# Kernel tuning notes

Hardware: AMD Instinct MI355X
Metric: run time of the kernel (lower is better)

The kernel has to match this reference:

```python
import jax, jax.numpy as jnp
import numpy as np

EMBED_DIM = 1024
NUM_HEADS = 16
HEAD_DIM = EMBED_DIM // NUM_HEADS
LAMBDA_ENTANGLE = 0.35


def setup_inputs() -> dict:
    key = jax.random.key(0)
    ks = jax.random.split(key, 10)
    B, S, D = 2, 2048, EMBED_DIM
    init = 1.0 / np.sqrt(D)  # mimic nn.Linear uniform init scale
    x = jax.random.normal(ks[0], (B, S, D), dtype=jnp.float32)
    Wq = jax.random.uniform(ks[1], (D, D), jnp.float32, -init, init)
    bq = jax.random.uniform(ks[2], (D,), jnp.float32, -init, init)
    Wk = jax.random.uniform(ks[3], (D, D), jnp.float32, -init, init)
    bk = jax.random.uniform(ks[4], (D,), jnp.float32, -init, init)
    Wv = jax.random.uniform(ks[5], (D, D), jnp.float32, -init, init)
    bv = jax.random.uniform(ks[6], (D,), jnp.float32, -init, init)
    Wo = jax.random.uniform(ks[7], (D, D), jnp.float32, -init, init)
    bo = jax.random.uniform(ks[8], (D,), jnp.float32, -init, init)
    J_attn = jax.random.normal(ks[9], (NUM_HEADS, HEAD_DIM, HEAD_DIM), dtype=jnp.float32) * 0.02
    lambda_attn = jnp.asarray(LAMBDA_ENTANGLE, dtype=jnp.float32)
    return {"x": x, "Wq": Wq, "bq": bq, "Wk": Wk, "bk": bk, "Wv": Wv, "bv": bv,
            "Wo": Wo, "bo": bo, "J_attn": J_attn, "lambda_attn": lambda_attn}


def reference(x, Wq, bq, Wk, bk, Wv, bv, Wo, bo, J_attn, lambda_attn):
    B, S, D = x.shape
    H, Hd = NUM_HEADS, HEAD_DIM
    scale = jnp.sqrt(jnp.asarray(Hd, dtype=x.dtype))

    def heads(W, b):
        # (B,S,D) @ (D,D) + b -> (B,H,S,Hd)
        y = jnp.einsum('bsd,ed->bse', x, W) + b
        return y.reshape(B, S, H, Hd).transpose(0, 2, 1, 3)

    Q = heads(Wq, bq)
    K = heads(Wk, bk)
    V = heads(Wv, bv)

    scores = jnp.einsum('bhid,bhjd->bhij', Q, K) / scale
    # bilinear entanglement correction: tanh(Q) J tanh(K)^T
    QJ = jnp.einsum('bhid,hde->bhie', jnp.tanh(Q), J_attn)  # (B,H,S,Hd)
    delta = jnp.einsum('bhie,bhje->bhij', QJ, jnp.tanh(K))
    scores = scores + lambda_attn * delta

    causal = jnp.triu(jnp.ones((S, S), dtype=bool), k=1)
    scores = jnp.where(causal, -jnp.inf, scores)

    probs = jax.nn.softmax(scores, axis=-1)
    out = jnp.einsum('bhij,bhjd->bhid', probs, V)  # (B,H,S,Hd)
    out = out.transpose(0, 2, 1, 3).reshape(B, S, D)
    return jnp.einsum('bsd,ed->bse', out, Wo) + bo
```

## Files before the change

kernel.cpp:

```cpp
#include <hip/hip_runtime.h>
#include <hip/hip_bf16.h>

typedef unsigned short u16;
typedef __bf16 bf16x8 __attribute__((ext_vector_type(8)));
typedef float f32x4 __attribute__((ext_vector_type(4)));
typedef unsigned short u16x4 __attribute__((ext_vector_type(4)));

#define MFMA16(a, b, c) __builtin_amdgcn_mfma_f32_16x16x32_bf16(a, b, c, 0, 0, 0)

#define EMB 1024
#define SEQ 2048
#define NH 16
#define HD 64
#define LOG2E 1.4426950408889634f

#define GLOAD_LDS16(g, l) __builtin_amdgcn_global_load_lds( \
    (const __attribute__((address_space(1))) unsigned int*)(g), \
    (__attribute__((address_space(3))) unsigned int*)(l), 16, 0, 0)

__device__ __forceinline__ float b2f(u16 u) {
    union { unsigned int i; float f; } v; v.i = ((unsigned int)u) << 16; return v.f;
}
__device__ __forceinline__ u16 f2b(float f) {
    __hip_bfloat16 h = __float2bfloat16(f);
    return *reinterpret_cast<u16*>(&h);
}
__device__ __forceinline__ u16x4 pack4(float a, float b, float c, float d) {
    union { __hip_bfloat162 h2[2]; u16x4 u; } r;
    r.h2[0] = __float22bfloat162_rn(float2{a, b});
    r.h2[1] = __float22bfloat162_rn(float2{c, d});
    return r.u;
}
__device__ __forceinline__ bf16x8 ldfrag(const u16* p) {
    return *reinterpret_cast<const bf16x8*>(p);
}
__device__ __forceinline__ bf16x8 cvt8(const float* p) {
    const float4 a = *reinterpret_cast<const float4*>(p);
    const float4 b = *reinterpret_cast<const float4*>(p + 4);
    union { u16x4 q[2]; bf16x8 v; } r;
    r.q[0] = pack4(a.x, a.y, a.z, a.w);
    r.q[1] = pack4(b.x, b.y, b.z, b.w);
    return r.v;
}
__device__ __forceinline__ float fast_tanh(float x) {
    float t = __builtin_amdgcn_exp2f(x * (2.0f * LOG2E));
    return 1.0f - 2.0f * __builtin_amdgcn_rcpf(t + 1.0f);
}
__device__ __forceinline__ bf16x8 tanh8(bf16x8 v) {
    union { bf16x8 v; u16 u[8]; } in; in.v = v;
    float o[8];
#pragma unroll
    for (int e = 0; e < 8; e++) o[e] = fast_tanh(b2f(in.u[e]));
    union { u16x4 q[2]; bf16x8 v; } r;
    r.q[0] = pack4(o[0], o[1], o[2], o[3]);
    r.q[1] = pack4(o[4], o[5], o[6], o[7]);
    return r.v;
}

__global__ __launch_bounds__(256) void cvt_all(
        const float* __restrict__ x,  const float* __restrict__ Wq,
        const float* __restrict__ Wk, const float* __restrict__ Wv,
        const float* __restrict__ Wo, u16* __restrict__ dst)
{
    size_t i = ((size_t)blockIdx.x * 256 + threadIdx.x) * 8;
    const float* src; size_t off;
    if (i < 4194304) { src = x; off = i; }
    else {
        size_t j = i - 4194304; int w = (int)(j >> 20); off = j & 1048575;
        src = (w == 0) ? Wq : (w == 1) ? Wk : (w == 2) ? Wv : Wo;
    }
    *(bf16x8*)&dst[i] = cvt8(src + off);
}

template<int MI>
__global__ __launch_bounds__(256, 4) void gemm_epi(
        const u16* __restrict__ A,
        const u16* __restrict__ W0, const float* __restrict__ B0,
        const u16* __restrict__ W1, const float* __restrict__ B1,
        const u16* __restrict__ W2, const float* __restrict__ B2,
        const float* __restrict__ lam,
        u16* __restrict__ Qa, u16* __restrict__ Ka, u16* __restrict__ Vt,
        float* __restrict__ out, int modeBase)
{
    const int mode = modeBase + blockIdx.z;
    const u16* W; const float* bias;
    if (blockIdx.z == 0)      { W = W0; bias = B0; }
    else if (blockIdx.z == 1) { W = W1; bias = B1; }
    else                      { W = W2; bias = B2; }

    __shared__ __attribute__((aligned(16))) u16 sA[MI * 32 * 64];
    __shared__ __attribute__((aligned(16))) u16 sB[128 * 64];

    const int t = threadIdx.x;
    const int w = t >> 6, L = t & 63;
    const int wm = w >> 1, wn = w & 1;
    const int lr = L & 15, lq = L >> 4;
    const int wbase = t & 192;
    const int m0 = blockIdx.y * (MI * 32), n0 = blockIdx.x * 128;

    f32x4 acc[MI][4];
#pragma unroll
    for (int i = 0; i < MI; i++)
#pragma unroll
        for (int j = 0; j < 4; j++) { f32x4 z = {0.f, 0.f, 0.f, 0.f}; acc[i][j] = z; }

    for (int k0 = 0; k0 < EMB; k0 += 64) {
        __syncthreads();
#pragma unroll
        for (int q = 0; q < MI; q++) {
            int c = q * 256 + t;
            int row = c >> 3, cc = c & 7;
            int col8 = cc ^ (row & 7);
            GLOAD_LDS16(&A[(size_t)(m0 + row) * EMB + k0 + col8 * 8],
                        &sA[(q * 256 + wbase) * 8]);
        }
#pragma unroll
        for (int q = 0; q < 4; q++) {
            int c = q * 256 + t;
            int row = c >> 3, cc = c & 7;
            int col8 = cc ^ (row & 7);
            GLOAD_LDS16(&W[(size_t)(n0 + row) * EMB + k0 + col8 * 8],
                        &sB[(q * 256 + wbase) * 8]);
        }
        __syncthreads();
#pragma unroll
        for (int s = 0; s < 2; s++) {
            bf16x8 af[MI], bfr[4];
#pragma unroll
            for (int mi = 0; mi < MI; mi++) {
                int row = wm * (MI * 16) + mi * 16 + lr;
                af[mi] = ldfrag(&sA[(row * 8 + ((s * 4 + lq) ^ (row & 7))) * 8]);
            }
#pragma unroll
            for (int ni = 0; ni < 4; ni++) {
                int row = wn * 64 + ni * 16 + lr;
                bfr[ni] = ldfrag(&sB[(row * 8 + ((s * 4 + lq) ^ (row & 7))) * 8]);
            }
#pragma unroll
            for (int mi = 0; mi < MI; mi++)
#pragma unroll
                for (int ni = 0; ni < 4; ni++)
                    acc[mi][ni] = MFMA16(af[mi], bfr[ni], acc[mi][ni]);
        }
    }

    const float lamf = lam[0];
#pragma unroll
    for (int mi = 0; mi < MI; mi++)
#pragma unroll
        for (int ni = 0; ni < 4; ni++) {
            int mb = m0 + wm * (MI * 16) + mi * 16 + lq * 4;
            int n  = n0 + wn * 64 + ni * 16 + lr;
            float bv = bias[n];
            if (mode == 3) {
#pragma unroll
                for (int r = 0; r < 4; r++)
                    out[(size_t)(mb + r) * EMB + n] = acc[mi][ni][r] + bv;
            } else {
                int b = mb >> 11, s0 = mb & 2047;
                int h = n >> 6,  d = n & 63;
                if (mode == 0) {
#pragma unroll
                    for (int r = 0; r < 4; r++) {
                        float val = acc[mi][ni][r] + bv;
                        size_t i128 = ((size_t)(b * NH + h) * SEQ + s0 + r) * 128 + d;
                        Qa[i128]      = f2b(val * (0.125f * LOG2E));
                        Qa[i128 + 64] = f2b(lamf * LOG2E * fast_tanh(val));
                    }
                } else if (mode == 1) {
#pragma unroll
                    for (int r = 0; r < 4; r++) {
                        float val = acc[mi][ni][r] + bv;
                        Ka[((size_t)(b * NH + h) * SEQ + s0 + r) * 128 + d] = f2b(val);
                    }
                } else {
                    u16x4 pk = pack4(acc[mi][ni][0] + bv, acc[mi][ni][1] + bv,
                                     acc[mi][ni][2] + bv, acc[mi][ni][3] + bv);
                    *(u16x4*)&Vt[((size_t)(b * NH + h) * HD + d) * SEQ + s0] = pk;
                }
            }
        }
}

__global__ __launch_bounds__(256) void ukern(
        const float* __restrict__ J, u16* __restrict__ Ka)
{
    __shared__ __attribute__((aligned(16))) u16 sJ[64 * 72];
    const int t = threadIdx.x, w = t >> 6, L = t & 63, lr = L & 15, lq = L >> 4;
    const int rt = blockIdx.x, bh = blockIdx.y, h = bh & 15;

#pragma unroll
    for (int i = 0; i < 2; i++) {
        int c = t + 256 * i;
        int row = c >> 3, col = (c & 7) * 8;
        *(bf16x8*)&sJ[row * 72 + col] = cvt8(&J[(size_t)h * 4096 + row * 64 + col]);
    }
    __syncthreads();

    const u16* krow = &Ka[((size_t)bh * SEQ + rt * 64 + w * 16 + lr) * 128];
    bf16x8 a0 = tanh8(ldfrag(krow + lq * 8));
    bf16x8 a1 = tanh8(ldfrag(krow + lq * 8 + 32));
#pragma unroll
    for (int nt = 0; nt < 4; nt++) {
        f32x4 acc = {0.f, 0.f, 0.f, 0.f};
        acc = MFMA16(a0, ldfrag(&sJ[(nt * 16 + lr) * 72 + lq * 8]), acc);
        acc = MFMA16(a1, ldfrag(&sJ[(nt * 16 + lr) * 72 + lq * 8 + 32]), acc);
#pragma unroll
        for (int r = 0; r < 4; r++) {
            int j = rt * 64 + w * 16 + lq * 4 + r;
            Ka[((size_t)bh * SEQ + j) * 128 + 64 + nt * 16 + lr] = f2b(acc[r]);
        }
    }
}

__global__ __launch_bounds__(512) void flash(
        const u16* __restrict__ Qa, const u16* __restrict__ Ka,
        const u16* __restrict__ Vt, u16* __restrict__ attn)
{
    __shared__ __attribute__((aligned(16))) u16 sK[2][64 * 128];
    __shared__ __attribute__((aligned(16))) u16 sVt[2][64 * 64];
    __shared__ __attribute__((aligned(16))) u16 sP[128 * 72];
    __shared__ float sLs[2][4][64][2];

    const int t = threadIdx.x, w = t >> 6, L = t & 63, lr = L & 15, lq = L >> 4;
    const int wq = w & 3, wk = w >> 2;
    const int bh = blockIdx.x & 31, p = blockIdx.x >> 5;
    const int i_l = wq * 16 + lr;
    const int wbase = t & 448;
    const u16* Kbase = Ka + (size_t)bh * SEQ * 128;
    const u16* Vbase = Vt + (size_t)bh * HD * SEQ;
    const int b = bh >> 4, h = bh & 15;
    float* sOt = reinterpret_cast<float*>(sK);

    auto stage = [&](int kn, int bsel) {
#pragma unroll
        for (int q = 0; q < 2; q++) {
            int cch = q * 512 + t;
            int row = cch >> 4, cc = cch & 15;
            int col8 = cc ^ (row & 15);
            GLOAD_LDS16(&Kbase[(size_t)(kn + row) * 128 + col8 * 8],
                        &sK[bsel][(q * 512 + wbase) * 8]);
        }
        {
            int d = t >> 3, cc = t & 7;
            int j8 = cc ^ (d & 7);
            GLOAD_LDS16(&Vbase[(size_t)d * SEQ + kn + j8 * 8],
                        &sVt[bsel][wbase * 8]);
        }
    };

#pragma unroll 1
    for (int seg = 0; seg < 2; seg++) {
        const int qt = seg ? 15 - p : p;
        const int qm = qt * 128;
        const int ktmax = 2 * qt + 1;

        bf16x8 qf[2][4];
#pragma unroll
        for (int g = 0; g < 2; g++) {
            const u16* qrow = Qa + ((size_t)bh * SEQ + qm + g * 64 + i_l) * 128;
#pragma unroll
            for (int s = 0; s < 4; s++) qf[g][s] = ldfrag(qrow + s * 32 + lq * 8);
        }

        f32x4 Ot[2][4];
#pragma unroll
        for (int g = 0; g < 2; g++)
#pragma unroll
            for (int i = 0; i < 4; i++) { f32x4 z = {0.f, 0.f, 0.f, 0.f}; Ot[g][i] = z; }
        float lsum[2] = {0.f, 0.f};

        stage(0, 0);
        __syncthreads();

        int cur = 0;
        for (int kt = 0; kt <= ktmax; kt++) {
            if (kt < ktmax) stage((kt + 1) * 64, cur ^ 1);
            const u16* sKc = sK[cur];
            const u16* sVc = sVt[cur];

            f32x4 sc[2][2];
#pragma unroll
            for (int g = 0; g < 2; g++)
#pragma unroll
                for (int m = 0; m < 2; m++) { f32x4 z = {0.f,0.f,0.f,0.f}; sc[g][m] = z; }
            __builtin_amdgcn_s_setprio(1);
#pragma unroll
            for (int mt2 = 0; mt2 < 2; mt2++) {
                int j = (wk * 2 + mt2) * 16 + lr;
#pragma unroll
                for (int s = 0; s < 4; s++) {
                    bf16x8 kf = ldfrag(&sKc[(j * 16 + ((s * 4 + lq) ^ (j & 15))) * 8]);
                    sc[0][mt2] = MFMA16(kf, qf[0][s], sc[0][mt2]);
                    sc[1][mt2] = MFMA16(kf, qf[1][s], sc[1][mt2]);
                }
            }
            __builtin_amdgcn_s_setprio(0);
            if (kt >= ktmax - 1) {
                const int thr0 = (kt == ktmax) ? -1  : i_l;
                const int thr1 = (kt == ktmax) ? i_l : 63;
#pragma unroll
                for (int mt2 = 0; mt2 < 2; mt2++)
#pragma unroll
                    for (int r = 0; r < 4; r++) {
                        int j = (wk * 2 + mt2) * 16 + lq * 4 + r;
                        if (j > thr0) sc[0][mt2][r] = -INFINITY;
                        if (j > thr1) sc[1][mt2][r] = -INFINITY;
                    }
            }
#pragma unroll
            for (int g = 0; g < 2; g++) {
#pragma unroll
                for (int mt2 = 0; mt2 < 2; mt2++) {
#pragma unroll
                    for (int r = 0; r < 4; r++) {
                        float e = __builtin_amdgcn_exp2f(sc[g][mt2][r]);
                        sc[g][mt2][r] = e;
                        lsum[g] += e;
                    }
                    *(u16x4*)&sP[(g * 64 + i_l) * 72 + (wk * 2 + mt2) * 16 + lq * 4] =
                        pack4(sc[g][mt2][0], sc[g][mt2][1], sc[g][mt2][2], sc[g][mt2][3]);
                }
            }
            __builtin_amdgcn_s_setprio(1);
            {
                bf16x8 pf0 = ldfrag(&sP[(i_l) * 72 + wk * 32 + lq * 8]);
                bf16x8 pf1 = ldfrag(&sP[(64 + i_l) * 72 + wk * 32 + lq * 8]);
#pragma unroll
                for (int mt = 0; mt < 4; mt++) {
                    int d = mt * 16 + lr;
                    bf16x8 vf = ldfrag(&sVc[(d * 8 + ((wk * 4 + lq) ^ (d & 7))) * 8]);
                    Ot[0][mt] = MFMA16(vf, pf0, Ot[0][mt]);
                    Ot[1][mt] = MFMA16(vf, pf1, Ot[1][mt]);
                }
            }
            __builtin_amdgcn_s_setprio(0);
            __syncthreads();
            cur ^= 1;
        }

#pragma unroll
        for (int g = 0; g < 2; g++) {
            lsum[g] += __shfl_xor(lsum[g], 16);
            lsum[g] += __shfl_xor(lsum[g], 32);
            sLs[wk][wq][L][g] = lsum[g];
        }
        if (wk == 1) {
            float* dst = &sOt[((size_t)wq * 64 + L) * 32];
#pragma unroll
            for (int g = 0; g < 2; g++)
#pragma unroll
                for (int mt = 0; mt < 4; mt++)
#pragma unroll
                    for (int r = 0; r < 4; r++)
                        dst[g * 16 + mt * 4 + r] = Ot[g][mt][r];
        }
        __syncthreads();
        if (wk == 0) {
            const float* src = &sOt[((size_t)wq * 64 + L) * 32];
#pragma unroll
            for (int g = 0; g < 2; g++) {
                float ls = lsum[g] + sLs[1][wq][L][g];
                const float r0 = __builtin_amdgcn_rcpf(ls);
                const float inv = r0 * (2.0f - ls * r0);
                const size_t base =
                    ((size_t)(b * SEQ + qm + g * 64 + i_l)) * EMB + h * HD;
#pragma unroll
                for (int mt = 0; mt < 4; mt++)
                    *(u16x4*)&attn[base + mt * 16 + lq * 4] = pack4(
                        (Ot[g][mt][0] + src[g * 16 + mt * 4 + 0]) * inv,
                        (Ot[g][mt][1] + src[g * 16 + mt * 4 + 1]) * inv,
                        (Ot[g][mt][2] + src[g * 16 + mt * 4 + 2]) * inv,
                        (Ot[g][mt][3] + src[g * 16 + mt * 4 + 3]) * inv);
            }
        }
        __syncthreads();
    }
}

extern "C" void kernel_launch(void* const* d_in, const int* in_sizes, int n_in,
                              void* d_out, int out_size, void* d_ws, size_t ws_size,
                              hipStream_t stream)
{
    const float* x   = (const float*)d_in[0];
    const float* Wq  = (const float*)d_in[1];
    const float* bq  = (const float*)d_in[2];
    const float* Wk  = (const float*)d_in[3];
    const float* bk  = (const float*)d_in[4];
    const float* Wv  = (const float*)d_in[5];
    const float* bv  = (const float*)d_in[6];
    const float* Wo  = (const float*)d_in[7];
    const float* bo  = (const float*)d_in[8];
    const float* J   = (const float*)d_in[9];
    const float* lam = (const float*)d_in[10];

    u16* ws  = (u16*)d_ws;
    u16* xb  = ws;
    u16* Wqb = xb  + (size_t)4096 * 1024;
    u16* Wkb = Wqb + (size_t)1024 * 1024;
    u16* Wvb = Wkb + (size_t)1024 * 1024;
    u16* Wob = Wvb + (size_t)1024 * 1024;
    u16* Qa  = Wob + (size_t)1024 * 1024;
    u16* Ka  = Qa  + (size_t)32 * 2048 * 128;
    u16* Vt  = Ka  + (size_t)32 * 2048 * 128;
    u16* attn = xb;
    float* dout = (float*)d_out;

    dim3 blk(256);
    cvt_all<<<dim3(4096), blk, 0, stream>>>(x, Wq, Wk, Wv, Wo, ws);
    gemm_epi<4><<<dim3(8, 32, 3), blk, 0, stream>>>(
        xb, Wqb, bq, Wkb, bk, Wvb, bv, lam, Qa, Ka, Vt, dout, 0);
    ukern<<<dim3(32, 32), blk, 0, stream>>>(J, Ka);
    flash<<<dim3(256), dim3(512), 0, stream>>>(Qa, Ka, Vt, attn);
    gemm_epi<2><<<dim3(8, 64, 1), blk, 0, stream>>>(
        attn, Wob, bo, Wob, bo, Wob, bo, lam, Qa, Ka, Vt, dout, 3);
}
```

Measured before the change: 196.7 us.

## Prefetch K/V tiles through registers instead of direct global-to-LDS loads

Replaces the global_load_lds async staging of the next K and V tiles with ordinary vector loads into registers, issued at the top of each iteration and written to the alternate LDS buffer after the PV MFMAs. Load addresses are precomputed once outside the loop. The exp/lsum code is rewritten to use separate temporaries with a tree sum. The cross-wave output reduction buffer in LDS is also changed to a strided transposed layout to avoid bank conflicts. This trades the async LDS-DMA path for extra registers and explicit ds_write instructions, which may raise register pressure at 512 threads.

```diff
diff --git a/kernel.cpp b/kernel.cpp
--- a/kernel.cpp
+++ b/kernel.cpp
@@ -226,28 +226,17 @@
     const int wq = w & 3, wk = w >> 2;
     const int bh = blockIdx.x & 31, p = blockIdx.x >> 5;
     const int i_l = wq * 16 + lr;
-    const int wbase = t & 448;
     const u16* Kbase = Ka + (size_t)bh * SEQ * 128;
     const u16* Vbase = Vt + (size_t)bh * HD * SEQ;
     const int b = bh >> 4, h = bh & 15;
     float* sOt = reinterpret_cast<float*>(sK);
 
-    auto stage = [&](int kn, int bsel) {
-#pragma unroll
-        for (int q = 0; q < 2; q++) {
-            int cch = q * 512 + t;
-            int row = cch >> 4, cc = cch & 15;
-            int col8 = cc ^ (row & 15);
-            GLOAD_LDS16(&Kbase[(size_t)(kn + row) * 128 + col8 * 8],
-                        &sK[bsel][(q * 512 + wbase) * 8]);
-        }
-        {
-            int d = t >> 3, cc = t & 7;
-            int j8 = cc ^ (d & 7);
-            GLOAD_LDS16(&Vbase[(size_t)d * SEQ + kn + j8 * 8],
-                        &sVt[bsel][wbase * 8]);
-        }
-    };
+    const int kr0 = t >> 4,        kc0 = (t & 15) ^ (kr0 & 15);
+    const int kr1 = (512 + t) >> 4, kc1 = (t & 15) ^ (kr1 & 15);
+    const int vd = t >> 3,          vj8 = (t & 7) ^ (vd & 7);
+    const u16* kq0 = Kbase + (size_t)kr0 * 128 + kc0 * 8;
+    const u16* kq1 = Kbase + (size_t)kr1 * 128 + kc1 * 8;
+    const u16* vq  = Vbase + (size_t)vd * SEQ + vj8 * 8;
 
 #pragma unroll 1
     for (int seg = 0; seg < 2; seg++) {
@@ -270,12 +259,26 @@
             for (int i = 0; i < 4; i++) { f32x4 z = {0.f, 0.f, 0.f, 0.f}; Ot[g][i] = z; }
         float lsum[2] = {0.f, 0.f};
 
-        stage(0, 0);
+        {
+            int4 rk0 = *(const int4*)kq0;
+            int4 rk1 = *(const int4*)kq1;
+            int4 rv  = *(const int4*)vq;
+            *(int4*)&sK[0][(size_t)t * 8]         = rk0;
+            *(int4*)&sK[0][(size_t)(512 + t) * 8] = rk1;
+            *(int4*)&sVt[0][(size_t)t * 8]        = rv;
+        }
         __syncthreads();
 
         int cur = 0;
         for (int kt = 0; kt <= ktmax; kt++) {
-            if (kt < ktmax) stage((kt + 1) * 64, cur ^ 1);
+            const bool pf = kt < ktmax;
+            int4 rk0, rk1, rv;
+            if (pf) {
+                const int kn = (kt + 1) * 64;
+                rk0 = *(const int4*)(kq0 + (size_t)kn * 128);
+                rk1 = *(const int4*)(kq1 + (size_t)kn * 128);
+                rv  = *(const int4*)(vq + kn);
+            }
             const u16* sKc = sK[cur];
             const u16* sVc = sVt[cur];
 
@@ -312,14 +315,13 @@
             for (int g = 0; g < 2; g++) {
 #pragma unroll
                 for (int mt2 = 0; mt2 < 2; mt2++) {
-#pragma unroll
-                    for (int r = 0; r < 4; r++) {
-                        float e = __builtin_amdgcn_exp2f(sc[g][mt2][r]);
-                        sc[g][mt2][r] = e;
-                        lsum[g] += e;
-                    }
+                    float e0 = __builtin_amdgcn_exp2f(sc[g][mt2][0]);
+                    float e1 = __builtin_amdgcn_exp2f(sc[g][mt2][1]);
+                    float e2 = __builtin_amdgcn_exp2f(sc[g][mt2][2]);
+                    float e3 = __builtin_amdgcn_exp2f(sc[g][mt2][3]);
+                    lsum[g] += (e0 + e1) + (e2 + e3);
                     *(u16x4*)&sP[(g * 64 + i_l) * 72 + (wk * 2 + mt2) * 16 + lq * 4] =
-                        pack4(sc[g][mt2][0], sc[g][mt2][1], sc[g][mt2][2], sc[g][mt2][3]);
+                        pack4(e0, e1, e2, e3);
                 }
             }
             __builtin_amdgcn_s_setprio(1);
@@ -335,6 +337,11 @@
                 }
             }
             __builtin_amdgcn_s_setprio(0);
+            if (pf) {
+                *(int4*)&sK[cur ^ 1][(size_t)t * 8]         = rk0;
+                *(int4*)&sK[cur ^ 1][(size_t)(512 + t) * 8] = rk1;
+                *(int4*)&sVt[cur ^ 1][(size_t)t * 8]        = rv;
+            }
             __syncthreads();
             cur ^= 1;
         }
@@ -346,18 +353,18 @@
             sLs[wk][wq][L][g] = lsum[g];
         }
         if (wk == 1) {
-            float* dst = &sOt[((size_t)wq * 64 + L) * 32];
+            float* dst = &sOt[wq * 64 + L];
 #pragma unroll
             for (int g = 0; g < 2; g++)
 #pragma unroll
                 for (int mt = 0; mt < 4; mt++)
 #pragma unroll
                     for (int r = 0; r < 4; r++)
-                        dst[g * 16 + mt * 4 + r] = Ot[g][mt][r];
+                        dst[256 * (g * 16 + mt * 4 + r)] = Ot[g][mt][r];
         }
         __syncthreads();
         if (wk == 0) {
-            const float* src = &sOt[((size_t)wq * 64 + L) * 32];
+            const float* src = &sOt[wq * 64 + L];
 #pragma unroll
             for (int g = 0; g < 2; g++) {
                 float ls = lsum[g] + sLs[1][wq][L][g];
@@ -368,10 +375,10 @@
 #pragma unroll
                 for (int mt = 0; mt < 4; mt++)
                     *(u16x4*)&attn[base + mt * 16 + lq * 4] = pack4(
-                        (Ot[g][mt][0] + src[g * 16 + mt * 4 + 0]) * inv,
-                        (Ot[g][mt][1] + src[g * 16 + mt * 4 + 1]) * inv,
-                        (Ot[g][mt][2] + src[g * 16 + mt * 4 + 2]) * inv,
-                        (Ot[g][mt][3] + src[g * 16 + mt * 4 + 3]) * inv);
+                        (Ot[g][mt][0] + src[256 * (g * 16 + mt * 4 + 0)]) * inv,
+                        (Ot[g][mt][1] + src[256 * (g * 16 + mt * 4 + 1)]) * inv,
+                        (Ot[g][mt][2] + src[256 * (g * 16 + mt * 4 + 2)]) * inv,
+                        (Ot[g][mt][3] + src[256 * (g * 16 + mt * 4 + 3)]) * inv);
             }
         }
         __syncthreads();
```

Measured after the change: 190.8 us. 3.0% less time.
